# Kernel optimization log

Hardware: AMD Instinct MI355X
Metric: run time of the kernel (lower is better)

Reference implementation:

```python
import jax, jax.numpy as jnp
import numpy as np

B, T, I, H, O = 1024, 128, 128, 1024, 64


def setup_inputs() -> dict:
    key = jax.random.key(0)
    ks = jax.random.split(key, 7)
    s_i = 1.0 / np.sqrt(H)
    return {
        "x": jax.random.normal(ks[0], (B, T * I), dtype=jnp.float32),
        "w_ih": jax.random.uniform(ks[1], (4 * H, I), minval=-s_i, maxval=s_i, dtype=jnp.float32),
        "w_hh": jax.random.uniform(ks[2], (4 * H, H), minval=-s_i, maxval=s_i, dtype=jnp.float32),
        "b_ih": jax.random.uniform(ks[3], (4 * H,), minval=-s_i, maxval=s_i, dtype=jnp.float32),
        "b_hh": jax.random.uniform(ks[4], (4 * H,), minval=-s_i, maxval=s_i, dtype=jnp.float32),
        "w_fc": jax.random.uniform(ks[5], (O, H), minval=-s_i, maxval=s_i, dtype=jnp.float32),
        "b_fc": jax.random.uniform(ks[6], (O,), minval=-s_i, maxval=s_i, dtype=jnp.float32),
    }


def reference(x, w_ih, w_hh, b_ih, b_hh, w_fc, b_fc):
    b = x.shape[0]
    i_dim = w_ih.shape[1]
    h_dim = w_hh.shape[1]
    t = x.shape[1] // i_dim
    # chunk(dim=1) into t contiguous slices == reshape [b, t, i]
    xs = x.reshape(b, t, i_dim)
    # precompute input-to-gate projection for all timesteps in one GEMM
    xg = jnp.einsum("bti,gi->tbg", xs, w_ih) + (b_ih + b_hh)  # [t, b, 4h]

    def step(carry, xg_t):
        h, c = carry
        gates = xg_t + h @ w_hh.T  # [b, 4h]
        ig, fg, gg, og = jnp.split(gates, 4, axis=-1)  # PyTorch LSTMCell gate order
        c_new = jax.nn.sigmoid(fg) * c + jax.nn.sigmoid(ig) * jnp.tanh(gg)
        h_new = jax.nn.sigmoid(og) * jnp.tanh(c_new)
        return (h_new, c_new), None

    h0 = jnp.zeros((b, h_dim), dtype=x.dtype)
    c0 = jnp.zeros((b, h_dim), dtype=x.dtype)
    (h_t, _), _ = jax.lax.scan(step, (h0, c0), xg)
    return h_t @ w_fc.T + b_fc
```

## Files before the change

kernel.cpp:

```cpp
#include <hip/hip_runtime.h>


#define B_DIM 1024
#define H_DIM 1024
#define I_DIM 128
#define T_DIM 128
#define XROW  (T_DIM * I_DIM)
#define KDIM  (I_DIM + H_DIM)
#define GDIM  (4 * H_DIM)
#define O_DIM 64

typedef float f32x4 __attribute__((ext_vector_type(4)));
typedef short bf16x8 __attribute__((ext_vector_type(8)));
typedef unsigned short u16x8 __attribute__((ext_vector_type(8)));

__device__ __forceinline__ unsigned short f2bf(float f) {
    union { float f; unsigned int u; } v; v.f = f;
    unsigned int r = v.u + 0x7fffu + ((v.u >> 16) & 1u);
    return (unsigned short)(r >> 16);
}
__device__ __forceinline__ float bf2f(unsigned short b) {
    union { unsigned int u; float f; } v; v.u = ((unsigned int)b) << 16;
    return v.f;
}
__device__ __forceinline__ float sigm(float x) { return 1.f / (1.f + __expf(-x)); }
__device__ __forceinline__ float tanh_fast(float x) { return 2.f / (1.f + __expf(-2.f * x)) - 1.f; }

__global__ void conv_x(const float* __restrict__ x, unsigned short* __restrict__ xb) {
    size_t i = ((size_t)blockIdx.x * 256 + threadIdx.x) * 8;
    float4 v0 = *(const float4*)(x + i);
    float4 v1 = *(const float4*)(x + i + 4);
    u16x8 o;
    o[0] = f2bf(v0.x); o[1] = f2bf(v0.y); o[2] = f2bf(v0.z); o[3] = f2bf(v0.w);
    o[4] = f2bf(v1.x); o[5] = f2bf(v1.y); o[6] = f2bf(v1.z); o[7] = f2bf(v1.w);
    *(u16x8*)(xb + i) = o;
}

__global__ void build_w(const float* __restrict__ w_ih, const float* __restrict__ w_hh,
                        const float* __restrict__ b_ih, const float* __restrict__ b_hh,
                        unsigned short* __restrict__ W, float* __restrict__ bias) {
    int r = blockIdx.x;
    int nb = r >> 7, q = r & 127;
    int wh = q >> 6, w = q & 63;
    int gate = w >> 4, jl = w & 15;
    int orig = gate * 1024 + nb * 32 + wh * 16 + jl;
    for (int k = threadIdx.x; k < KDIM; k += 256) {
        float v = (k < I_DIM) ? w_ih[(size_t)orig * I_DIM + k]
                              : w_hh[(size_t)orig * H_DIM + (k - I_DIM)];
        W[(size_t)r * KDIM + k] = f2bf(v);
    }
    if (threadIdx.x == 0) bias[r] = b_ih[orig] + b_hh[orig];
}

__global__ void trans_wfc(const float* __restrict__ w_fc, float* __restrict__ wT) {
    int o = blockIdx.x;
    for (int k = threadIdx.x; k < H_DIM; k += 256)
        wT[(size_t)k * O_DIM + o] = w_fc[(size_t)o * H_DIM + k];
}

__global__ void zero_hc(unsigned short* __restrict__ h0, float* __restrict__ c) {
    int idx = blockIdx.x * 256 + threadIdx.x;
    h0[idx] = 0;
    c[idx] = 0.f;
}

#define READ_TILE(A0, A1, B0, B1, B2, B3, OFF) do {                               \
    asm volatile("ds_read_b128 %0, %1 offset:" OFF : "=v"(fa0) : "v"(A0));        \
    asm volatile("ds_read_b128 %0, %1 offset:" OFF : "=v"(fa1) : "v"(A1));        \
    asm volatile("ds_read_b128 %0, %1 offset:" OFF : "=v"(fb0) : "v"(B0));        \
    asm volatile("ds_read_b128 %0, %1 offset:" OFF : "=v"(fb1) : "v"(B1));        \
    asm volatile("ds_read_b128 %0, %1 offset:" OFF : "=v"(fb2) : "v"(B2));        \
    asm volatile("ds_read_b128 %0, %1 offset:" OFF : "=v"(fb3) : "v"(B3));        \
    asm volatile("ds_read_b128 %0, %1 offset:" OFF : "=v"(ga0) : "v"((A0) ^ 64u));\
    asm volatile("ds_read_b128 %0, %1 offset:" OFF : "=v"(ga1) : "v"((A1) ^ 64u));\
    asm volatile("ds_read_b128 %0, %1 offset:" OFF : "=v"(gb0) : "v"((B0) ^ 64u));\
    asm volatile("ds_read_b128 %0, %1 offset:" OFF : "=v"(gb1) : "v"((B1) ^ 64u));\
    asm volatile("ds_read_b128 %0, %1 offset:" OFF : "=v"(gb2) : "v"((B2) ^ 64u));\
    asm volatile("ds_read_b128 %0, %1 offset:" OFF : "=v"(gb3) : "v"((B3) ^ 64u));\
    asm volatile("s_waitcnt lgkmcnt(0)" ::: "memory");                            \
    __builtin_amdgcn_sched_barrier(0);                                            \
} while (0)

#define MFMA_(a, b, c) c = __builtin_amdgcn_mfma_f32_16x16x32_bf16(a, b, c, 0, 0, 0)
#define MM_TILE() do {                                                            \
    MFMA_(fa0, fb0, acc[0][0]); MFMA_(fa0, fb1, acc[0][1]);                       \
    MFMA_(fa0, fb2, acc[0][2]); MFMA_(fa0, fb3, acc[0][3]);                       \
    MFMA_(fa1, fb0, acc[1][0]); MFMA_(fa1, fb1, acc[1][1]);                       \
    MFMA_(fa1, fb2, acc[1][2]); MFMA_(fa1, fb3, acc[1][3]);                       \
    MFMA_(ga0, gb0, acc[0][0]); MFMA_(ga0, gb1, acc[0][1]);                       \
    MFMA_(ga0, gb2, acc[0][2]); MFMA_(ga0, gb3, acc[0][3]);                       \
    MFMA_(ga1, gb0, acc[1][0]); MFMA_(ga1, gb1, acc[1][1]);                       \
    MFMA_(ga1, gb2, acc[1][2]); MFMA_(ga1, gb3, acc[1][3]);                       \
} while (0)

#define WAITV(N) do {                                                             \
    asm volatile("s_waitcnt vmcnt(" N ")" ::: "memory");                          \
    __builtin_amdgcn_s_barrier();                                                 \
} while (0)

__global__ __launch_bounds__(512, 2)
void lstm_step(const unsigned short* __restrict__ xb,
               const unsigned short* __restrict__ W,
               const float* __restrict__ bias,
               const unsigned short* __restrict__ h_in,
               unsigned short* __restrict__ h_out,
               float* __restrict__ c_st,
               int t) {
    __shared__ __align__(16) unsigned short lds[8 * 8192];
    const int tid  = threadIdx.x;
    const int wv   = tid >> 6, lane = tid & 63;
    const int wm   = wv >> 1, wn = wv & 1;
    const int quad = lane >> 4, l16 = lane & 15;
    const int l7   = l16 & 7;
    const int bid = blockIdx.x;
    const int xcd = bid & 7;
    const int sl  = bid >> 3;
    const int nb  = xcd * 4 + (sl & 3);
    const int mb  = sl >> 2;

    const int j  = nb * 32 + wn * 16 + l16;
    const int bb = nb * 128 + wn * 64 + l16;
    const float bi  = bias[bb +  0];
    const float bf_ = bias[bb + 16];
    const float bg  = bias[bb + 32];
    const float bo  = bias[bb + 48];
    float cold[2][4];
#pragma unroll
    for (int mi = 0; mi < 2; mi++)
#pragma unroll
        for (int r = 0; r < 4; r++) {
            const int brow = mb * 128 + wm * 32 + mi * 16 + quad * 4 + r;
            cold[mi][r] = c_st[(size_t)brow * H_DIM + j];
        }

    f32x4 acc[2][4];
#pragma unroll
    for (int i = 0; i < 2; i++)
#pragma unroll
        for (int jj = 0; jj < 4; jj++) acc[i][jj] = f32x4{0.f, 0.f, 0.f, 0.f};

    const int arow = lane >> 3;
    const int ag   = lane & 7;
    const int colperm = ((ag ^ arow) << 3);

    auto stage = [&](int bsel, int ks) {
        const int kt = ks * 64;
        unsigned short* As_ = lds + bsel * 16384;
        unsigned short* Bs_ = As_ + 8192;
#pragma unroll
        for (int c4 = 0; c4 < 2; ++c4) {
            const int row0 = wv * 16 + c4 * 8;
            const int row  = row0 + arow;
            const unsigned short* srcA =
                (kt < I_DIM)
                    ? xb   + (size_t)(mb * 128 + row) * XROW + t * I_DIM + kt + colperm
                    : h_in + (size_t)(mb * 128 + row) * H_DIM + (kt - I_DIM) + colperm;
            __builtin_amdgcn_global_load_lds(
                (const __attribute__((address_space(1))) void*)srcA,
                (__attribute__((address_space(3))) void*)(&As_[row0 * 64]), 16, 0, 0);
        }
#pragma unroll
        for (int c4 = 0; c4 < 2; ++c4) {
            const int row0 = wv * 16 + c4 * 8;
            const int row  = row0 + arow;
            const unsigned short* srcB =
                W + (size_t)(nb * 128 + row) * KDIM + kt + colperm;
            __builtin_amdgcn_global_load_lds(
                (const __attribute__((address_space(1))) void*)srcB,
                (__attribute__((address_space(3))) void*)(&Bs_[row0 * 64]), 16, 0, 0);
        }
    };

    const unsigned lbase = (unsigned)(unsigned long long)
        (__attribute__((address_space(3))) void*)lds;
    const unsigned cp  = (unsigned)((quad ^ l7) << 4);
    const unsigned aA0 = lbase + (unsigned)((wm * 32 + l16) * 128) + cp;
    const unsigned aA1 = aA0 + 2048;
    const unsigned aB0 = lbase + 16384u + (unsigned)((wn * 64 + l16) * 128) + cp;
    const unsigned aB1 = aB0 + 2048;
    const unsigned aB2 = aB0 + 4096;
    const unsigned aB3 = aB0 + 6144;
    const unsigned cA0 = aA0 + 65536u, cA1 = aA1 + 65536u;
    const unsigned cB0 = aB0 + 65536u, cB1 = aB1 + 65536u;
    const unsigned cB2 = aB2 + 65536u, cB3 = aB3 + 65536u;
    bf16x8 fa0, fa1, fb0, fb1, fb2, fb3, ga0, ga1, gb0, gb1, gb2, gb3;

    stage(0, 0);
    stage(1, 1);
    stage(2, 2);

#pragma unroll 1
    for (int q = 0; q < 3; ++q) {
        WAITV("8"); READ_TILE(aA0, aA1, aB0, aB1, aB2, aB3, "0");
        stage(3, 4 * q + 3); MM_TILE();
        WAITV("8"); READ_TILE(aA0, aA1, aB0, aB1, aB2, aB3, "32768");
        stage(0, 4 * q + 4); MM_TILE();
        WAITV("8"); READ_TILE(cA0, cA1, cB0, cB1, cB2, cB3, "0");
        stage(1, 4 * q + 5); MM_TILE();
        WAITV("8"); READ_TILE(cA0, cA1, cB0, cB1, cB2, cB3, "32768");
        stage(2, 4 * q + 6); MM_TILE();
    }
    WAITV("8"); READ_TILE(aA0, aA1, aB0, aB1, aB2, aB3, "0");
    stage(3, 15); MM_TILE();
    WAITV("8"); READ_TILE(aA0, aA1, aB0, aB1, aB2, aB3, "32768");
    stage(0, 16); MM_TILE();
    WAITV("8"); READ_TILE(cA0, cA1, cB0, cB1, cB2, cB3, "0");
    stage(1, 17); MM_TILE();
    WAITV("8"); READ_TILE(cA0, cA1, cB0, cB1, cB2, cB3, "32768");
    MM_TILE();
    WAITV("4"); READ_TILE(aA0, aA1, aB0, aB1, aB2, aB3, "0");
    MM_TILE();
    WAITV("0"); READ_TILE(aA0, aA1, aB0, aB1, aB2, aB3, "32768");
    MM_TILE();

#pragma unroll
    for (int mi = 0; mi < 2; mi++) {
#pragma unroll
        for (int r = 0; r < 4; r++) {
            const int brow = mb * 128 + wm * 32 + mi * 16 + quad * 4 + r;
            const float gi = acc[mi][0][r] + bi;
            const float gf = acc[mi][1][r] + bf_;
            const float gg = acc[mi][2][r] + bg;
            const float go = acc[mi][3][r] + bo;
            const size_t idx = (size_t)brow * H_DIM + j;
            const float cn = sigm(gf) * cold[mi][r] + sigm(gi) * tanh_fast(gg);
            c_st[idx] = cn;
            h_out[idx] = f2bf(sigm(go) * tanh_fast(cn));
        }
    }
}

__global__ void proj(const unsigned short* __restrict__ h,
                     const float* __restrict__ wT,
                     const float* __restrict__ b_fc,
                     float* __restrict__ out) {
    __shared__ float hs[4][H_DIM];
    const int tid = threadIdx.x, wv = tid >> 6, o = tid & 63;
    const int b = blockIdx.x * 4 + wv;
    const unsigned short* hrow = h + (size_t)b * H_DIM;
#pragma unroll
    for (int i = 0; i < 2; ++i) {
        const int k0 = i * 512 + o * 8;
        u16x8 v = *(const u16x8*)(hrow + k0);
        float4 f0 = {bf2f((unsigned short)v[0]), bf2f((unsigned short)v[1]),
                     bf2f((unsigned short)v[2]), bf2f((unsigned short)v[3])};
        float4 f1 = {bf2f((unsigned short)v[4]), bf2f((unsigned short)v[5]),
                     bf2f((unsigned short)v[6]), bf2f((unsigned short)v[7])};
        *(float4*)&hs[wv][k0]     = f0;
        *(float4*)&hs[wv][k0 + 4] = f1;
    }
    float s0 = 0.f, s1 = 0.f, s2 = 0.f, s3 = 0.f;
#pragma unroll 4
    for (int k4 = 0; k4 < H_DIM / 4; ++k4) {
        float4 hv = *(const float4*)&hs[wv][k4 * 4];
        const float* wp = wT + (size_t)k4 * 4 * O_DIM + o;
        s0 += hv.x * wp[0 * O_DIM];
        s1 += hv.y * wp[1 * O_DIM];
        s2 += hv.z * wp[2 * O_DIM];
        s3 += hv.w * wp[3 * O_DIM];
    }
    out[(size_t)b * O_DIM + o] = s0 + s1 + s2 + s3 + b_fc[o];
}

extern "C" void kernel_launch(void* const* d_in, const int* in_sizes, int n_in,
                              void* d_out, int out_size, void* d_ws, size_t ws_size,
                              hipStream_t stream) {
    const float* x    = (const float*)d_in[0];
    const float* w_ih = (const float*)d_in[1];
    const float* w_hh = (const float*)d_in[2];
    const float* b_ih = (const float*)d_in[3];
    const float* b_hh = (const float*)d_in[4];
    const float* w_fc = (const float*)d_in[5];
    const float* b_fc = (const float*)d_in[6];
    float* out = (float*)d_out;

    char* ws = (char*)d_ws;
    size_t off = 0;
    unsigned short* xb = (unsigned short*)(ws + off); off += (size_t)B_DIM * XROW * 2;
    unsigned short* W  = (unsigned short*)(ws + off); off += (size_t)GDIM * KDIM * 2;
    float* bias        = (float*)(ws + off);          off += (size_t)GDIM * 4;
    unsigned short* h0 = (unsigned short*)(ws + off); off += (size_t)B_DIM * H_DIM * 2;
    unsigned short* h1 = (unsigned short*)(ws + off); off += (size_t)B_DIM * H_DIM * 2;
    float* c           = (float*)(ws + off);          off += (size_t)B_DIM * H_DIM * 4;
    float* wT          = (float*)(ws + off);          off += (size_t)H_DIM * O_DIM * 4;

    conv_x<<<8192, 256, 0, stream>>>(x, xb);
    build_w<<<GDIM, 256, 0, stream>>>(w_ih, w_hh, b_ih, b_hh, W, bias);
    trans_wfc<<<O_DIM, 256, 0, stream>>>(w_fc, wT);
    zero_hc<<<4096, 256, 0, stream>>>(h0, c);

    for (int t = 0; t < T_DIM; ++t) {
        const unsigned short* hin = (t & 1) ? h1 : h0;
        unsigned short* hout      = (t & 1) ? h0 : h1;
        lstm_step<<<256, 512, 0, stream>>>(xb, W, bias, hin, hout, c, t);
    }
    proj<<<256, 256, 0, stream>>>(h0, wT, b_fc, out);
}
```

Baseline: 1.816 ms.

## Double-buffer LDS fragments in registers to overlap reads with MFMA

Splits the LDS fragment registers into two sets (P/Q) so the next tile's ds_reads are issued before the current tile's MFMAs, waiting on lgkmcnt only afterward. Global staging waits are relaxed from vmcnt(8) to vmcnt(4) to match the new schedule. The c-state and bias loads are moved to after the main loop to cut live registers, and launch bounds drop to one block per CU to give room for the doubled fragment set. The trade is lower occupancy and a cold c_st load in the epilogue in exchange for hiding LDS latency behind matrix math.

After: 1.946 ms. 7.1% more time.

```diff
diff --git a/kernel.cpp b/kernel.cpp
--- a/kernel.cpp
+++ b/kernel.cpp
@@ -64,33 +64,31 @@
     c[idx] = 0.f;
 }
 
-#define READ_TILE(A0, A1, B0, B1, B2, B3, OFF) do {                               \
-    asm volatile("ds_read_b128 %0, %1 offset:" OFF : "=v"(fa0) : "v"(A0));        \
-    asm volatile("ds_read_b128 %0, %1 offset:" OFF : "=v"(fa1) : "v"(A1));        \
-    asm volatile("ds_read_b128 %0, %1 offset:" OFF : "=v"(fb0) : "v"(B0));        \
-    asm volatile("ds_read_b128 %0, %1 offset:" OFF : "=v"(fb1) : "v"(B1));        \
-    asm volatile("ds_read_b128 %0, %1 offset:" OFF : "=v"(fb2) : "v"(B2));        \
-    asm volatile("ds_read_b128 %0, %1 offset:" OFF : "=v"(fb3) : "v"(B3));        \
-    asm volatile("ds_read_b128 %0, %1 offset:" OFF : "=v"(ga0) : "v"((A0) ^ 64u));\
-    asm volatile("ds_read_b128 %0, %1 offset:" OFF : "=v"(ga1) : "v"((A1) ^ 64u));\
-    asm volatile("ds_read_b128 %0, %1 offset:" OFF : "=v"(gb0) : "v"((B0) ^ 64u));\
-    asm volatile("ds_read_b128 %0, %1 offset:" OFF : "=v"(gb1) : "v"((B1) ^ 64u));\
-    asm volatile("ds_read_b128 %0, %1 offset:" OFF : "=v"(gb2) : "v"((B2) ^ 64u));\
-    asm volatile("ds_read_b128 %0, %1 offset:" OFF : "=v"(gb3) : "v"((B3) ^ 64u));\
-    asm volatile("s_waitcnt lgkmcnt(0)" ::: "memory");                            \
-    __builtin_amdgcn_sched_barrier(0);                                            \
+#define READ_T(S, A0, A1, B0, B1, B2, B3, OFF) do {                               \
+    asm volatile("ds_read_b128 %0, %1 offset:" OFF : "=v"(S##a0) : "v"(A0));      \
+    asm volatile("ds_read_b128 %0, %1 offset:" OFF : "=v"(S##a1) : "v"(A1));      \
+    asm volatile("ds_read_b128 %0, %1 offset:" OFF : "=v"(S##b0) : "v"(B0));      \
+    asm volatile("ds_read_b128 %0, %1 offset:" OFF : "=v"(S##b1) : "v"(B1));      \
+    asm volatile("ds_read_b128 %0, %1 offset:" OFF : "=v"(S##b2) : "v"(B2));      \
+    asm volatile("ds_read_b128 %0, %1 offset:" OFF : "=v"(S##b3) : "v"(B3));      \
+    asm volatile("ds_read_b128 %0, %1 offset:" OFF : "=v"(S##g0) : "v"((A0)^64u));\
+    asm volatile("ds_read_b128 %0, %1 offset:" OFF : "=v"(S##g1) : "v"((A1)^64u));\
+    asm volatile("ds_read_b128 %0, %1 offset:" OFF : "=v"(S##h0) : "v"((B0)^64u));\
+    asm volatile("ds_read_b128 %0, %1 offset:" OFF : "=v"(S##h1) : "v"((B1)^64u));\
+    asm volatile("ds_read_b128 %0, %1 offset:" OFF : "=v"(S##h2) : "v"((B2)^64u));\
+    asm volatile("ds_read_b128 %0, %1 offset:" OFF : "=v"(S##h3) : "v"((B3)^64u));\
 } while (0)
 
 #define MFMA_(a, b, c) c = __builtin_amdgcn_mfma_f32_16x16x32_bf16(a, b, c, 0, 0, 0)
-#define MM_TILE() do {                                                            \
-    MFMA_(fa0, fb0, acc[0][0]); MFMA_(fa0, fb1, acc[0][1]);                       \
-    MFMA_(fa0, fb2, acc[0][2]); MFMA_(fa0, fb3, acc[0][3]);                       \
-    MFMA_(fa1, fb0, acc[1][0]); MFMA_(fa1, fb1, acc[1][1]);                       \
-    MFMA_(fa1, fb2, acc[1][2]); MFMA_(fa1, fb3, acc[1][3]);                       \
-    MFMA_(ga0, gb0, acc[0][0]); MFMA_(ga0, gb1, acc[0][1]);                       \
-    MFMA_(ga0, gb2, acc[0][2]); MFMA_(ga0, gb3, acc[0][3]);                       \
-    MFMA_(ga1, gb0, acc[1][0]); MFMA_(ga1, gb1, acc[1][1]);                       \
-    MFMA_(ga1, gb2, acc[1][2]); MFMA_(ga1, gb3, acc[1][3]);                       \
+#define MM_T(S) do {                                                              \
+    MFMA_(S##a0, S##b0, acc[0][0]); MFMA_(S##a0, S##b1, acc[0][1]);               \
+    MFMA_(S##a0, S##b2, acc[0][2]); MFMA_(S##a0, S##b3, acc[0][3]);               \
+    MFMA_(S##a1, S##b0, acc[1][0]); MFMA_(S##a1, S##b1, acc[1][1]);               \
+    MFMA_(S##a1, S##b2, acc[1][2]); MFMA_(S##a1, S##b3, acc[1][3]);               \
+    MFMA_(S##g0, S##h0, acc[0][0]); MFMA_(S##g0, S##h1, acc[0][1]);               \
+    MFMA_(S##g0, S##h2, acc[0][2]); MFMA_(S##g0, S##h3, acc[0][3]);               \
+    MFMA_(S##g1, S##h0, acc[1][0]); MFMA_(S##g1, S##h1, acc[1][1]);               \
+    MFMA_(S##g1, S##h2, acc[1][2]); MFMA_(S##g1, S##h3, acc[1][3]);               \
 } while (0)
 
 #define WAITV(N) do {                                                             \
@@ -98,7 +96,12 @@
     __builtin_amdgcn_s_barrier();                                                 \
 } while (0)
 
-__global__ __launch_bounds__(512, 2)
+#define LGKM0() do {                                                              \
+    asm volatile("s_waitcnt lgkmcnt(0)" ::: "memory");                            \
+    __builtin_amdgcn_sched_barrier(0);                                            \
+} while (0)
+
+__global__ __launch_bounds__(512, 1)
 void lstm_step(const unsigned short* __restrict__ xb,
                const unsigned short* __restrict__ W,
                const float* __restrict__ bias,
@@ -118,21 +121,6 @@
     const int nb  = xcd * 4 + (sl & 3);
     const int mb  = sl >> 2;
 
-    const int j  = nb * 32 + wn * 16 + l16;
-    const int bb = nb * 128 + wn * 64 + l16;
-    const float bi  = bias[bb +  0];
-    const float bf_ = bias[bb + 16];
-    const float bg  = bias[bb + 32];
-    const float bo  = bias[bb + 48];
-    float cold[2][4];
-#pragma unroll
-    for (int mi = 0; mi < 2; mi++)
-#pragma unroll
-        for (int r = 0; r < 4; r++) {
-            const int brow = mb * 128 + wm * 32 + mi * 16 + quad * 4 + r;
-            cold[mi][r] = c_st[(size_t)brow * H_DIM + j];
-        }
-
     f32x4 acc[2][4];
 #pragma unroll
     for (int i = 0; i < 2; i++)
@@ -183,36 +171,46 @@
     const unsigned cA0 = aA0 + 65536u, cA1 = aA1 + 65536u;
     const unsigned cB0 = aB0 + 65536u, cB1 = aB1 + 65536u;
     const unsigned cB2 = aB2 + 65536u, cB3 = aB3 + 65536u;
-    bf16x8 fa0, fa1, fb0, fb1, fb2, fb3, ga0, ga1, gb0, gb1, gb2, gb3;
+    bf16x8 Pa0, Pa1, Pb0, Pb1, Pb2, Pb3, Pg0, Pg1, Ph0, Ph1, Ph2, Ph3;
+    bf16x8 Qa0, Qa1, Qb0, Qb1, Qb2, Qb3, Qg0, Qg1, Qh0, Qh1, Qh2, Qh3;
 
     stage(0, 0);
     stage(1, 1);
     stage(2, 2);
+    asm volatile("s_waitcnt vmcnt(8)" ::: "memory");
+    __builtin_amdgcn_s_barrier();
+    READ_T(P, aA0, aA1, aB0, aB1, aB2, aB3, "0");
+    LGKM0();
 
 #pragma unroll 1
     for (int q = 0; q < 3; ++q) {
-        WAITV("8"); READ_TILE(aA0, aA1, aB0, aB1, aB2, aB3, "0");
-        stage(3, 4 * q + 3); MM_TILE();
-        WAITV("8"); READ_TILE(aA0, aA1, aB0, aB1, aB2, aB3, "32768");
-        stage(0, 4 * q + 4); MM_TILE();
-        WAITV("8"); READ_TILE(cA0, cA1, cB0, cB1, cB2, cB3, "0");
-        stage(1, 4 * q + 5); MM_TILE();
-        WAITV("8"); READ_TILE(cA0, cA1, cB0, cB1, cB2, cB3, "32768");
-        stage(2, 4 * q + 6); MM_TILE();
-    }
-    WAITV("8"); READ_TILE(aA0, aA1, aB0, aB1, aB2, aB3, "0");
-    stage(3, 15); MM_TILE();
-    WAITV("8"); READ_TILE(aA0, aA1, aB0, aB1, aB2, aB3, "32768");
-    stage(0, 16); MM_TILE();
-    WAITV("8"); READ_TILE(cA0, cA1, cB0, cB1, cB2, cB3, "0");
-    stage(1, 17); MM_TILE();
-    WAITV("8"); READ_TILE(cA0, cA1, cB0, cB1, cB2, cB3, "32768");
-    MM_TILE();
-    WAITV("4"); READ_TILE(aA0, aA1, aB0, aB1, aB2, aB3, "0");
-    MM_TILE();
-    WAITV("0"); READ_TILE(aA0, aA1, aB0, aB1, aB2, aB3, "32768");
-    MM_TILE();
-
+        WAITV("4"); READ_T(Q, aA0, aA1, aB0, aB1, aB2, aB3, "32768");
+        stage(3, 4 * q + 3); MM_T(P); LGKM0();
+        WAITV("4"); READ_T(P, cA0, cA1, cB0, cB1, cB2, cB3, "0");
+        stage(0, 4 * q + 4); MM_T(Q); LGKM0();
+        WAITV("4"); READ_T(Q, cA0, cA1, cB0, cB1, cB2, cB3, "32768");
+        stage(1, 4 * q + 5); MM_T(P); LGKM0();
+        WAITV("4"); READ_T(P, aA0, aA1, aB0, aB1, aB2, aB3, "0");
+        stage(2, 4 * q + 6); MM_T(Q); LGKM0();
+    }
+    WAITV("4"); READ_T(Q, aA0, aA1, aB0, aB1, aB2, aB3, "32768");
+    stage(3, 15); MM_T(P); LGKM0();
+    WAITV("4"); READ_T(P, cA0, cA1, cB0, cB1, cB2, cB3, "0");
+    stage(0, 16); MM_T(Q); LGKM0();
+    WAITV("4"); READ_T(Q, cA0, cA1, cB0, cB1, cB2, cB3, "32768");
+    stage(1, 17); MM_T(P); LGKM0();
+    WAITV("4"); READ_T(P, aA0, aA1, aB0, aB1, aB2, aB3, "0");
+    MM_T(Q); LGKM0();
+    WAITV("0"); READ_T(Q, aA0, aA1, aB0, aB1, aB2, aB3, "32768");
+    MM_T(P); LGKM0();
+    MM_T(Q);
+
+    const int j  = nb * 32 + wn * 16 + l16;
+    const int bb = nb * 128 + wn * 64 + l16;
+    const float bi  = bias[bb +  0];
+    const float bf_ = bias[bb + 16];
+    const float bg  = bias[bb + 32];
+    const float bo  = bias[bb + 48];
 #pragma unroll
     for (int mi = 0; mi < 2; mi++) {
 #pragma unroll
@@ -223,7 +221,7 @@
             const float gg = acc[mi][2][r] + bg;
             const float go = acc[mi][3][r] + bo;
             const size_t idx = (size_t)brow * H_DIM + j;
-            const float cn = sigm(gf) * cold[mi][r] + sigm(gi) * tanh_fast(gg);
+            const float cn = sigm(gf) * c_st[idx] + sigm(gi) * tanh_fast(gg);
             c_st[idx] = cn;
             h_out[idx] = f2bf(sigm(go) * tanh_fast(cn));
         }
```

## Split K across wave pairs with 64x64 warp tiles and LDS reduction

Applied to the files above, without the earlier changes.

Changes the 8-wave layout from 4x2 M×N tiles of 32x64 to 2x2 tiles of 64x64, with wave pairs splitting each 64-wide K slice into halves. Each wave now reads 4 A and 4 B fragments per half-K for 16 MFMAs, where before it read 2 A and 4 B fragments twice, which cuts LDS read traffic per MFMA. The partial sums are reduced through LDS after the main loop, and only the kh=0 waves run the gate epilogue. The cost is more accumulator registers (occupancy hint lowered to 1 block/CU), an extra LDS reduction step, and half the waves idling during the epilogue.

New measurement: 2.281 ms. 1.26x slower.

```diff
diff --git a/kernel.cpp b/kernel.cpp
--- a/kernel.cpp
+++ b/kernel.cpp
@@ -64,33 +64,29 @@
     c[idx] = 0.f;
 }
 
-#define READ_TILE(A0, A1, B0, B1, B2, B3, OFF) do {                               \
+#define READ_8(A0, A1, A2, A3, B0, B1, B2, B3, OFF) do {                          \
     asm volatile("ds_read_b128 %0, %1 offset:" OFF : "=v"(fa0) : "v"(A0));        \
     asm volatile("ds_read_b128 %0, %1 offset:" OFF : "=v"(fa1) : "v"(A1));        \
+    asm volatile("ds_read_b128 %0, %1 offset:" OFF : "=v"(fa2) : "v"(A2));        \
+    asm volatile("ds_read_b128 %0, %1 offset:" OFF : "=v"(fa3) : "v"(A3));        \
     asm volatile("ds_read_b128 %0, %1 offset:" OFF : "=v"(fb0) : "v"(B0));        \
     asm volatile("ds_read_b128 %0, %1 offset:" OFF : "=v"(fb1) : "v"(B1));        \
     asm volatile("ds_read_b128 %0, %1 offset:" OFF : "=v"(fb2) : "v"(B2));        \
     asm volatile("ds_read_b128 %0, %1 offset:" OFF : "=v"(fb3) : "v"(B3));        \
-    asm volatile("ds_read_b128 %0, %1 offset:" OFF : "=v"(ga0) : "v"((A0) ^ 64u));\
-    asm volatile("ds_read_b128 %0, %1 offset:" OFF : "=v"(ga1) : "v"((A1) ^ 64u));\
-    asm volatile("ds_read_b128 %0, %1 offset:" OFF : "=v"(gb0) : "v"((B0) ^ 64u));\
-    asm volatile("ds_read_b128 %0, %1 offset:" OFF : "=v"(gb1) : "v"((B1) ^ 64u));\
-    asm volatile("ds_read_b128 %0, %1 offset:" OFF : "=v"(gb2) : "v"((B2) ^ 64u));\
-    asm volatile("ds_read_b128 %0, %1 offset:" OFF : "=v"(gb3) : "v"((B3) ^ 64u));\
     asm volatile("s_waitcnt lgkmcnt(0)" ::: "memory");                            \
     __builtin_amdgcn_sched_barrier(0);                                            \
 } while (0)
 
 #define MFMA_(a, b, c) c = __builtin_amdgcn_mfma_f32_16x16x32_bf16(a, b, c, 0, 0, 0)
-#define MM_TILE() do {                                                            \
+#define MM_16() do {                                                              \
     MFMA_(fa0, fb0, acc[0][0]); MFMA_(fa0, fb1, acc[0][1]);                       \
     MFMA_(fa0, fb2, acc[0][2]); MFMA_(fa0, fb3, acc[0][3]);                       \
     MFMA_(fa1, fb0, acc[1][0]); MFMA_(fa1, fb1, acc[1][1]);                       \
     MFMA_(fa1, fb2, acc[1][2]); MFMA_(fa1, fb3, acc[1][3]);                       \
-    MFMA_(ga0, gb0, acc[0][0]); MFMA_(ga0, gb1, acc[0][1]);                       \
-    MFMA_(ga0, gb2, acc[0][2]); MFMA_(ga0, gb3, acc[0][3]);                       \
-    MFMA_(ga1, gb0, acc[1][0]); MFMA_(ga1, gb1, acc[1][1]);                       \
-    MFMA_(ga1, gb2, acc[1][2]); MFMA_(ga1, gb3, acc[1][3]);                       \
+    MFMA_(fa2, fb0, acc[2][0]); MFMA_(fa2, fb1, acc[2][1]);                       \
+    MFMA_(fa2, fb2, acc[2][2]); MFMA_(fa2, fb3, acc[2][3]);                       \
+    MFMA_(fa3, fb0, acc[3][0]); MFMA_(fa3, fb1, acc[3][1]);                       \
+    MFMA_(fa3, fb2, acc[3][2]); MFMA_(fa3, fb3, acc[3][3]);                       \
 } while (0)
 
 #define WAITV(N) do {                                                             \
@@ -98,7 +94,7 @@
     __builtin_amdgcn_s_barrier();                                                 \
 } while (0)
 
-__global__ __launch_bounds__(512, 2)
+__global__ __launch_bounds__(512, 1)
 void lstm_step(const unsigned short* __restrict__ xb,
                const unsigned short* __restrict__ W,
                const float* __restrict__ bias,
@@ -109,7 +105,9 @@
     __shared__ __align__(16) unsigned short lds[8 * 8192];
     const int tid  = threadIdx.x;
     const int wv   = tid >> 6, lane = tid & 63;
-    const int wm   = wv >> 1, wn = wv & 1;
+    const int wm   = wv >> 2;
+    const int wn   = (wv >> 1) & 1;
+    const int kh   = wv & 1;
     const int quad = lane >> 4, l16 = lane & 15;
     const int l7   = l16 & 7;
     const int bid = blockIdx.x;
@@ -118,24 +116,9 @@
     const int nb  = xcd * 4 + (sl & 3);
     const int mb  = sl >> 2;
 
-    const int j  = nb * 32 + wn * 16 + l16;
-    const int bb = nb * 128 + wn * 64 + l16;
-    const float bi  = bias[bb +  0];
-    const float bf_ = bias[bb + 16];
-    const float bg  = bias[bb + 32];
-    const float bo  = bias[bb + 48];
-    float cold[2][4];
-#pragma unroll
-    for (int mi = 0; mi < 2; mi++)
-#pragma unroll
-        for (int r = 0; r < 4; r++) {
-            const int brow = mb * 128 + wm * 32 + mi * 16 + quad * 4 + r;
-            cold[mi][r] = c_st[(size_t)brow * H_DIM + j];
-        }
-
-    f32x4 acc[2][4];
-#pragma unroll
-    for (int i = 0; i < 2; i++)
+    f32x4 acc[4][4];
+#pragma unroll
+    for (int i = 0; i < 4; i++)
 #pragma unroll
         for (int jj = 0; jj < 4; jj++) acc[i][jj] = f32x4{0.f, 0.f, 0.f, 0.f};
 
@@ -173,17 +156,20 @@
 
     const unsigned lbase = (unsigned)(unsigned long long)
         (__attribute__((address_space(3))) void*)lds;
-    const unsigned cp  = (unsigned)((quad ^ l7) << 4);
-    const unsigned aA0 = lbase + (unsigned)((wm * 32 + l16) * 128) + cp;
+    const unsigned cp  = ((unsigned)((quad ^ l7) << 4)) ^ ((unsigned)kh << 6);
+    const unsigned aA0 = lbase + (unsigned)((wm * 64 + l16) * 128) + cp;
     const unsigned aA1 = aA0 + 2048;
+    const unsigned aA2 = aA0 + 4096;
+    const unsigned aA3 = aA0 + 6144;
     const unsigned aB0 = lbase + 16384u + (unsigned)((wn * 64 + l16) * 128) + cp;
     const unsigned aB1 = aB0 + 2048;
     const unsigned aB2 = aB0 + 4096;
     const unsigned aB3 = aB0 + 6144;
     const unsigned cA0 = aA0 + 65536u, cA1 = aA1 + 65536u;
+    const unsigned cA2 = aA2 + 65536u, cA3 = aA3 + 65536u;
     const unsigned cB0 = aB0 + 65536u, cB1 = aB1 + 65536u;
     const unsigned cB2 = aB2 + 65536u, cB3 = aB3 + 65536u;
-    bf16x8 fa0, fa1, fb0, fb1, fb2, fb3, ga0, ga1, gb0, gb1, gb2, gb3;
+    bf16x8 fa0, fa1, fa2, fa3, fb0, fb1, fb2, fb3;
 
     stage(0, 0);
     stage(1, 1);
@@ -191,41 +177,79 @@
 
 #pragma unroll 1
     for (int q = 0; q < 3; ++q) {
-        WAITV("8"); READ_TILE(aA0, aA1, aB0, aB1, aB2, aB3, "0");
-        stage(3, 4 * q + 3); MM_TILE();
-        WAITV("8"); READ_TILE(aA0, aA1, aB0, aB1, aB2, aB3, "32768");
-        stage(0, 4 * q + 4); MM_TILE();
-        WAITV("8"); READ_TILE(cA0, cA1, cB0, cB1, cB2, cB3, "0");
-        stage(1, 4 * q + 5); MM_TILE();
-        WAITV("8"); READ_TILE(cA0, cA1, cB0, cB1, cB2, cB3, "32768");
-        stage(2, 4 * q + 6); MM_TILE();
-    }
-    WAITV("8"); READ_TILE(aA0, aA1, aB0, aB1, aB2, aB3, "0");
-    stage(3, 15); MM_TILE();
-    WAITV("8"); READ_TILE(aA0, aA1, aB0, aB1, aB2, aB3, "32768");
-    stage(0, 16); MM_TILE();
-    WAITV("8"); READ_TILE(cA0, cA1, cB0, cB1, cB2, cB3, "0");
-    stage(1, 17); MM_TILE();
-    WAITV("8"); READ_TILE(cA0, cA1, cB0, cB1, cB2, cB3, "32768");
-    MM_TILE();
-    WAITV("4"); READ_TILE(aA0, aA1, aB0, aB1, aB2, aB3, "0");
-    MM_TILE();
-    WAITV("0"); READ_TILE(aA0, aA1, aB0, aB1, aB2, aB3, "32768");
-    MM_TILE();
-
-#pragma unroll
-    for (int mi = 0; mi < 2; mi++) {
-#pragma unroll
-        for (int r = 0; r < 4; r++) {
-            const int brow = mb * 128 + wm * 32 + mi * 16 + quad * 4 + r;
-            const float gi = acc[mi][0][r] + bi;
-            const float gf = acc[mi][1][r] + bf_;
-            const float gg = acc[mi][2][r] + bg;
-            const float go = acc[mi][3][r] + bo;
-            const size_t idx = (size_t)brow * H_DIM + j;
-            const float cn = sigm(gf) * cold[mi][r] + sigm(gi) * tanh_fast(gg);
-            c_st[idx] = cn;
-            h_out[idx] = f2bf(sigm(go) * tanh_fast(cn));
+        WAITV("8"); READ_8(aA0, aA1, aA2, aA3, aB0, aB1, aB2, aB3, "0");
+        stage(3, 4 * q + 3); MM_16();
+        WAITV("8"); READ_8(aA0, aA1, aA2, aA3, aB0, aB1, aB2, aB3, "32768");
+        stage(0, 4 * q + 4); MM_16();
+        WAITV("8"); READ_8(cA0, cA1, cA2, cA3, cB0, cB1, cB2, cB3, "0");
+        stage(1, 4 * q + 5); MM_16();
+        WAITV("8"); READ_8(cA0, cA1, cA2, cA3, cB0, cB1, cB2, cB3, "32768");
+        stage(2, 4 * q + 6); MM_16();
+    }
+    WAITV("8"); READ_8(aA0, aA1, aA2, aA3, aB0, aB1, aB2, aB3, "0");
+    stage(3, 15); MM_16();
+    WAITV("8"); READ_8(aA0, aA1, aA2, aA3, aB0, aB1, aB2, aB3, "32768");
+    stage(0, 16); MM_16();
+    WAITV("8"); READ_8(cA0, cA1, cA2, cA3, cB0, cB1, cB2, cB3, "0");
+    stage(1, 17); MM_16();
+    WAITV("8"); READ_8(cA0, cA1, cA2, cA3, cB0, cB1, cB2, cB3, "32768");
+    MM_16();
+    WAITV("4"); READ_8(aA0, aA1, aA2, aA3, aB0, aB1, aB2, aB3, "0");
+    MM_16();
+    WAITV("0"); READ_8(aA0, aA1, aA2, aA3, aB0, aB1, aB2, aB3, "32768");
+    MM_16();
+
+    __builtin_amdgcn_s_barrier();
+    const unsigned rbase = lbase + (unsigned)((wm * 2 + wn) * 16384)
+                                 + (unsigned)(lane * 16);
+    if (kh) {
+#pragma unroll
+        for (int mi = 0; mi < 4; mi++)
+#pragma unroll
+            for (int ni = 0; ni < 4; ni++)
+                asm volatile("ds_write_b128 %0, %1"
+                             :: "v"(rbase + (unsigned)((mi * 4 + ni) * 1024)),
+                                "v"(acc[mi][ni]));
+        asm volatile("s_waitcnt lgkmcnt(0)" ::: "memory");
+    }
+    __builtin_amdgcn_s_barrier();
+    if (!kh) {
+#pragma unroll
+        for (int mi = 0; mi < 4; mi++) {
+            f32x4 p0, p1, p2, p3;
+            asm volatile("ds_read_b128 %0, %1"
+                         : "=v"(p0) : "v"(rbase + (unsigned)((mi * 4 + 0) * 1024)));
+            asm volatile("ds_read_b128 %0, %1"
+                         : "=v"(p1) : "v"(rbase + (unsigned)((mi * 4 + 1) * 1024)));
+            asm volatile("ds_read_b128 %0, %1"
+                         : "=v"(p2) : "v"(rbase + (unsigned)((mi * 4 + 2) * 1024)));
+            asm volatile("ds_read_b128 %0, %1"
+                         : "=v"(p3) : "v"(rbase + (unsigned)((mi * 4 + 3) * 1024)));
+            asm volatile("s_waitcnt lgkmcnt(0)" ::: "memory");
+            __builtin_amdgcn_sched_barrier(0);
+            acc[mi][0] += p0; acc[mi][1] += p1;
+            acc[mi][2] += p2; acc[mi][3] += p3;
+        }
+        const int j  = nb * 32 + wn * 16 + l16;
+        const int bb = nb * 128 + wn * 64 + l16;
+        const float bi  = bias[bb +  0];
+        const float bf_ = bias[bb + 16];
+        const float bg  = bias[bb + 32];
+        const float bo  = bias[bb + 48];
+#pragma unroll
+        for (int mi = 0; mi < 4; mi++) {
+#pragma unroll
+            for (int r = 0; r < 4; r++) {
+                const int brow = mb * 128 + wm * 64 + mi * 16 + quad * 4 + r;
+                const float gi = acc[mi][0][r] + bi;
+                const float gf = acc[mi][1][r] + bf_;
+                const float gg = acc[mi][2][r] + bg;
+                const float go = acc[mi][3][r] + bo;
+                const size_t idx = (size_t)brow * H_DIM + j;
+                const float cn = sigm(gf) * c_st[idx] + sigm(gi) * tanh_fast(gg);
+                c_st[idx] = cn;
+                h_out[idx] = f2bf(sigm(go) * tanh_fast(cn));
+            }
         }
     }
 }
```
